# Performance work log

Measured on AMD Instinct MI355X. Metric: run time of the kernel, lower is better.

## Reference

```python
import jax, jax.numpy as jnp
import numpy as np

N_TOKEN = 32000
N_LAYER = 6
N_HEAD = 16
D_MODEL = 1024
D_HEAD = 64
D_INNER = 4096
QLEN = 512
MEM_LEN = 512
BSZ = 8
HD = N_HEAD * D_HEAD
SCALE = 1.0 / float(np.sqrt(D_HEAD))
NEG = -1e30


def _layer_norm(x, g, b, eps=1e-5):
    mu = jnp.mean(x, axis=-1, keepdims=True)
    var = jnp.var(x, axis=-1, keepdims=True)
    return (x - mu) * jax.lax.rsqrt(var + eps) * g + b


def _rel_shift(x):
    # x: [qlen, klen, bsz, n_head] -- TXL relative-position shift
    q, k, b, n = x.shape
    zp = jnp.zeros((q, 1, b, n), x.dtype)
    xp = jnp.concatenate([zp, x], axis=1).reshape(k + 1, q, b, n)
    return xp[1:].reshape(q, k, b, n)


def setup_inputs():
    key = jax.random.key(0)
    ks = jax.random.split(key, 12)
    s = 0.02
    rn = lambda k, *sh: jax.random.normal(k, sh, jnp.float32) * s
    z = lambda *sh: jnp.zeros(sh, jnp.float32)
    o = lambda *sh: jnp.ones(sh, jnp.float32)
    return {
        "data": jax.random.randint(ks[0], (QLEN, BSZ), 0, N_TOKEN),
        "target": jax.random.randint(ks[1], (QLEN, BSZ), 0, N_TOKEN),
        "memory": jax.random.normal(ks[2], (N_LAYER, MEM_LEN, BSZ, D_MODEL), jnp.float32),
        "emb_W": rn(ks[3], N_TOKEN, D_MODEL),  # tied input embedding / softmax head
        "r_w_bias": rn(ks[4], N_HEAD, D_HEAD),
        "r_r_bias": rn(ks[5], N_HEAD, D_HEAD),
        "Wq": rn(ks[6], N_LAYER, D_MODEL, HD),
        "Wkv": rn(ks[7], N_LAYER, D_MODEL, 2 * HD),
        "Wr": rn(ks[8], N_LAYER, D_MODEL, HD),
        "Wo": rn(ks[9], N_LAYER, HD, D_MODEL),
        "W1": rn(ks[10], N_LAYER, D_MODEL, D_INNER),
        "b1": z(N_LAYER, D_INNER),
        "W2": rn(ks[11], N_LAYER, D_INNER, D_MODEL),
        "b2": z(N_LAYER, D_MODEL),
        "ln1_g": o(N_LAYER, D_MODEL),
        "ln1_b": z(N_LAYER, D_MODEL),
        "ln2_g": o(N_LAYER, D_MODEL),
        "ln2_b": z(N_LAYER, D_MODEL),
    }


def _model(data, target, memory, emb_W, r_w_bias, r_r_bias, Wq, Wkv, Wr, Wo,
           W1, b1, W2, b2, ln1_g, ln1_b, ln2_g, ln2_b):
    qlen, bsz = data.shape
    mem = jax.lax.stop_gradient(memory)  # TXL detaches memories
    mlen = mem.shape[1]
    klen = mlen + qlen

    word_emb = emb_W[data]  # [q, b, d]

    # sinusoidal relative positions klen-1 .. 0
    pos_seq = jnp.arange(klen - 1, -1, -1, dtype=word_emb.dtype)
    inv_freq = 1.0 / (10000.0 ** (jnp.arange(0, D_MODEL, 2, dtype=word_emb.dtype) / D_MODEL))
    sin_inp = pos_seq[:, None] * inv_freq[None, :]
    pos = jnp.concatenate([jnp.sin(sin_inp), jnp.cos(sin_inp)], axis=-1)  # [klen, d]

    # causal mask with memory: query i can attend keys j <= i + mlen
    mask = jnp.arange(klen)[None, :] > (jnp.arange(qlen)[:, None] + mlen)  # [q, k]

    core = word_emb
    hids = [core]
    for i in range(N_LAYER):
        x_mem = jnp.concatenate([mem[i], core], axis=0)  # [klen, b, d]
        q = (core @ Wq[i]).reshape(qlen, bsz, N_HEAD, D_HEAD)
        kv = x_mem @ Wkv[i]
        k, v = jnp.split(kv, 2, axis=-1)
        k = k.reshape(klen, bsz, N_HEAD, D_HEAD)
        v = v.reshape(klen, bsz, N_HEAD, D_HEAD)
        r_k = (pos @ Wr[i]).reshape(klen, N_HEAD, D_HEAD)

        AC = jnp.einsum('ibnd,jbnd->ijbn', q + r_w_bias, k)
        BD = _rel_shift(jnp.einsum('ibnd,jnd->ijbn', q + r_r_bias, r_k))
        score = (AC + BD) * SCALE
        score = jnp.where(mask[:, :, None, None], NEG, score)
        prob = jax.nn.softmax(score, axis=1)
        vec = jnp.einsum('ijbn,jbnd->ibnd', prob, v).reshape(qlen, bsz, HD)
        attn_out = vec @ Wo[i]
        core = _layer_norm(core + attn_out, ln1_g[i], ln1_b[i])
        ff = jax.nn.relu(core @ W1[i] + b1[i]) @ W2[i] + b2[i]
        core = _layer_norm(core + ff, ln2_g[i], ln2_b[i])
        hids.append(core)

    # adaptive softmax with cutoffs=[] == full tied softmax
    logits = core @ emb_W.T  # [q, b, V]
    logp = jax.nn.log_softmax(logits, axis=-1)
    loss = -jnp.take_along_axis(logp, target[..., None], axis=-1)[..., 0]  # [q, b]

    new_mems = jnp.stack([
        jnp.concatenate([mem[i], hids[i]], axis=0)[-MEM_LEN:] for i in range(N_LAYER)
    ])
    new_mems = jax.lax.stop_gradient(new_mems)
    return loss, new_mems


def reference(data, target, memory, emb_W, r_w_bias, r_r_bias, Wq, Wkv, Wr, Wo,
              W1, b1, W2, b2, ln1_g, ln1_b, ln2_g, ln2_b):
    return _model(data, target, memory, emb_W, r_w_bias, r_r_bias, Wq, Wkv, Wr, Wo,
                  W1, b1, W2, b2, ln1_g, ln1_b, ln2_g, ln2_b)
```

## Files before the change

kernel.cpp:

```cpp
#include <hip/hip_runtime.h>
#include <hip/hip_bf16.h>
#include <math.h>

#define QLEN   512
#define MLEN   512
#define KLEN   1024
#define BSZ    8
#define NH     16
#define DH     64
#define DM     1024
#define DI     4096
#define NTOK   32000
#define NROW   4096
#define XROW   8192
#define VTILES 500

typedef __hip_bfloat16 bf16;
typedef __attribute__((ext_vector_type(8))) short bf16x8;
typedef __attribute__((ext_vector_type(4))) float f32x4;

__device__ __forceinline__ unsigned short f2b(float x) {
    union { float f; unsigned u; } a; a.f = x;
    unsigned r = a.u + 0x7fffu + ((a.u >> 16) & 1u);
    return (unsigned short)(r >> 16);
}
__device__ __forceinline__ float b2f(unsigned short h) {
    union { unsigned u; float f; } a; a.u = ((unsigned)h) << 16;
    return a.f;
}

__device__ __forceinline__ void gload_lds16(const void* g, void* l) {
    __builtin_amdgcn_global_load_lds(
        (const __attribute__((address_space(1))) unsigned int*)g,
        (__attribute__((address_space(3))) unsigned int*)l, 16, 0, 0);
}

__global__ __launch_bounds__(256) void posb_kernel(unsigned short* __restrict__ posb) {
    int j = blockIdx.x;
    int t = threadIdx.x;
    float p = (float)(1023 - j);
    #pragma unroll
    for (int u = 0; u < 4; u++) {
        int dcol = t + u * 256;
        int k = dcol & 511;
        float invf = expf(-((float)k) * (1.0f / 512.0f) * 9.210340371976184f);
        float a = p * invf;
        posb[j * DM + dcol] = f2b((dcol < 512) ? sinf(a) : cosf(a));
    }
}

__global__ __launch_bounds__(256) void gather_emb(const int* __restrict__ data,
                                                  const float* __restrict__ emb,
                                                  float* __restrict__ out) {
    int row = blockIdx.x;
    int t = threadIdx.x;
    int tok = data[row];
    const float4* src = (const float4*)(emb + (size_t)tok * DM);
    float4* dst = (float4*)(out + (size_t)row * DM);
    dst[t] = src[t];
}

__global__ __launch_bounds__(256) void cast_bf16(const float* __restrict__ src,
                                                 unsigned short* __restrict__ dst, int n4) {
    int i = blockIdx.x * 256 + threadIdx.x;
    if (i < n4) {
        float4 v = ((const float4*)src)[i];
        ushort4 o;
        o.x = f2b(v.x); o.y = f2b(v.y); o.z = f2b(v.z); o.w = f2b(v.w);
        ((ushort4*)dst)[i] = o;
    }
}

__global__ __launch_bounds__(256) void castT_kernel(const float* __restrict__ src,
                                                    unsigned short* __restrict__ dst,
                                                    int K, int N) {
    __shared__ float T[32][33];
    int t = threadIdx.x;
    int k0 = blockIdx.y * 32, n0 = blockIdx.x * 32;
    int r = t >> 3, c4 = (t & 7) * 4;
    float4 v = *(const float4*)(src + (size_t)(k0 + r) * N + n0 + c4);
    T[r][c4 + 0] = v.x; T[r][c4 + 1] = v.y; T[r][c4 + 2] = v.z; T[r][c4 + 3] = v.w;
    __syncthreads();
    ushort4 o;
    o.x = f2b(T[c4 + 0][r]); o.y = f2b(T[c4 + 1][r]);
    o.z = f2b(T[c4 + 2][r]); o.w = f2b(T[c4 + 3][r]);
    *(ushort4*)(dst + (size_t)(n0 + r) * K + k0 + c4) = o;
}

template <bool BIAS, bool RELU, bool OUTBF16>
__global__ __launch_bounds__(256) void gemm_bt(const unsigned short* __restrict__ A,
                                               const unsigned short* __restrict__ B,
                                               const float* __restrict__ bias,
                                               void* __restrict__ Cout,
                                               int M, int N, int K) {
    __shared__ unsigned short As[128 * 32];
    __shared__ unsigned short Bs[128 * 32];
    int t = threadIdx.x;
    int wave = t >> 6, lane = t & 63;
    int bm = blockIdx.y * 128, bn = blockIdx.x * 128;
    int wm = (wave >> 1) * 64, wn = (wave & 1) * 64;
    int quad = lane >> 4, l16 = lane & 15;

    f32x4 acc[4][4] = {};

    int srow = wave * 32 + (lane >> 2);
    int scol = (lane & 3) * 8;
    const unsigned short* Ag = A + (size_t)(bm + srow) * K + scol;
    const unsigned short* Bg = B + (size_t)(bn + srow) * K + scol;
    unsigned short* Al0 = As + (wave * 32) * 32;
    unsigned short* Al1 = As + (wave * 32 + 16) * 32;
    unsigned short* Bl0 = Bs + (wave * 32) * 32;
    unsigned short* Bl1 = Bs + (wave * 32 + 16) * 32;

    for (int kt = 0; kt < K; kt += 32) {
        gload_lds16(Ag + kt, Al0);
        gload_lds16(Ag + kt + (size_t)16 * K, Al1);
        gload_lds16(Bg + kt, Bl0);
        gload_lds16(Bg + kt + (size_t)16 * K, Bl1);
        __syncthreads();
        bf16x8 af[4], bfr[4];
        #pragma unroll
        for (int mi = 0; mi < 4; mi++)
            af[mi] = *(const bf16x8*)&As[(wm + mi * 16 + l16) * 32 + quad * 8];
        #pragma unroll
        for (int ni = 0; ni < 4; ni++)
            bfr[ni] = *(const bf16x8*)&Bs[(wn + ni * 16 + l16) * 32 + quad * 8];
        #pragma unroll
        for (int mi = 0; mi < 4; mi++)
            #pragma unroll
            for (int ni = 0; ni < 4; ni++)
                acc[mi][ni] = __builtin_amdgcn_mfma_f32_16x16x32_bf16(
                    af[mi], bfr[ni], acc[mi][ni], 0, 0, 0);
        __syncthreads();
    }

    #pragma unroll
    for (int mi = 0; mi < 4; mi++) {
        #pragma unroll
        for (int ni = 0; ni < 4; ni++) {
            int c = bn + wn + ni * 16 + l16;
            float bv = BIAS ? bias[c] : 0.0f;
            #pragma unroll
            for (int reg = 0; reg < 4; reg++) {
                int r = bm + wm + mi * 16 + quad * 4 + reg;
                float x = acc[mi][ni][reg];
                if (BIAS) x += bv;
                if (RELU) x = fmaxf(x, 0.0f);
                if (OUTBF16) ((unsigned short*)Cout)[(size_t)r * N + c] = f2b(x);
                else         ((float*)Cout)[(size_t)r * N + c] = x;
            }
        }
    }
}

__global__ __launch_bounds__(256) void lse_gemm_mfma(const unsigned short* __restrict__ A,
                                                     const unsigned short* __restrict__ B,
                                                     float* __restrict__ pmax,
                                                     float* __restrict__ psum) {
    __shared__ unsigned short As[128 * 32];
    __shared__ unsigned short Bs[128 * 32];
    int t = threadIdx.x;
    int wave = t >> 6, lane = t & 63;
    int bm = blockIdx.y * 128, bn = blockIdx.x * 128;
    int wm = (wave >> 1) * 64;
    int quad = lane >> 4, l16 = lane & 15;
    const int K = 1024;

    f32x4 acc[4][4] = {};

    int srow = wave * 32 + (lane >> 2);
    int scol = (lane & 3) * 8;
    const unsigned short* Ag = A + (size_t)(bm + srow) * K + scol;
    const unsigned short* Bg = B + (size_t)(bn + srow) * K + scol;
    unsigned short* Al0 = As + (wave * 32) * 32;
    unsigned short* Al1 = As + (wave * 32 + 16) * 32;
    unsigned short* Bl0 = Bs + (wave * 32) * 32;
    unsigned short* Bl1 = Bs + (wave * 32 + 16) * 32;
    int wn = (wave & 1) * 64;

    for (int kt = 0; kt < K; kt += 32) {
        gload_lds16(Ag + kt, Al0);
        gload_lds16(Ag + kt + (size_t)16 * K, Al1);
        gload_lds16(Bg + kt, Bl0);
        gload_lds16(Bg + kt + (size_t)16 * K, Bl1);
        __syncthreads();
        bf16x8 af[4], bfr[4];
        #pragma unroll
        for (int mi = 0; mi < 4; mi++)
            af[mi] = *(const bf16x8*)&As[(wm + mi * 16 + l16) * 32 + quad * 8];
        #pragma unroll
        for (int ni = 0; ni < 4; ni++)
            bfr[ni] = *(const bf16x8*)&Bs[(wn + ni * 16 + l16) * 32 + quad * 8];
        #pragma unroll
        for (int mi = 0; mi < 4; mi++)
            #pragma unroll
            for (int ni = 0; ni < 4; ni++)
                acc[mi][ni] = __builtin_amdgcn_mfma_f32_16x16x32_bf16(
                    af[mi], bfr[ni], acc[mi][ni], 0, 0, 0);
        __syncthreads();
    }

    int vt = blockIdx.x * 2 + (wave & 1);
    #pragma unroll
    for (int mi = 0; mi < 4; mi++) {
        #pragma unroll
        for (int reg = 0; reg < 4; reg++) {
            float m = -1e30f;
            #pragma unroll
            for (int ni = 0; ni < 4; ni++) m = fmaxf(m, acc[mi][ni][reg]);
            #pragma unroll
            for (int off = 1; off < 16; off <<= 1) m = fmaxf(m, __shfl_xor(m, off, 64));
            float s = 0.0f;
            #pragma unroll
            for (int ni = 0; ni < 4; ni++) s += __expf(acc[mi][ni][reg] - m);
            #pragma unroll
            for (int off = 1; off < 16; off <<= 1) s += __shfl_xor(s, off, 64);
            if (l16 == 0) {
                int r = bm + wm + mi * 16 + quad * 4 + reg;
                pmax[(size_t)r * VTILES + vt] = m;
                psum[(size_t)r * VTILES + vt] = s;
            }
        }
    }
}

__global__ __launch_bounds__(256) void qprep(const float* __restrict__ qbuf,
                                             const float* __restrict__ rwb,
                                             const float* __restrict__ rrb,
                                             unsigned short* __restrict__ qw,
                                             unsigned short* __restrict__ qr) {
    int row = blockIdx.x;
    int t = threadIdx.x;
    int i = row >> 3;
    float4 v = ((const float4*)(qbuf + (size_t)row * DM))[t];
    float4 w = ((const float4*)rwb)[t];
    float4 r = ((const float4*)rrb)[t];
    ushort4 ow, os;
    ow.x = f2b(v.x + w.x); ow.y = f2b(v.y + w.y); ow.z = f2b(v.z + w.z); ow.w = f2b(v.w + w.w);
    os.x = f2b(v.x + r.x); os.y = f2b(v.y + r.y); os.z = f2b(v.z + r.z); os.w = f2b(v.w + r.w);
    ((ushort4*)(qr + (size_t)row * DM))[t] = os;
    int col = t * 4;
    int idx = (col & ~63) + ((col & 63) ^ ((i & 7) << 3));
    *(ushort4*)(qw + (size_t)row * DM + idx) = ow;
}

__global__ __launch_bounds__(256) void kvprep(const float* __restrict__ kvf,
                                              unsigned short* __restrict__ Kh,
                                              unsigned short* __restrict__ Vth) {
    int nb = blockIdx.x, jt = blockIdx.y;
    int n = nb >> 3, b = nb & 7;
    int t = threadIdx.x;
    __shared__ float T[64][65];
    int jj = t >> 2, c4 = (t & 3) * 16;
    int j = jt * 64 + jj;
    const float* src = kvf + (size_t)(j * 8 + b) * 2048 + n * 64;
    unsigned short* kdst = Kh + (size_t)nb * 65536 + (size_t)j * 64;
    #pragma unroll
    for (int c = 0; c < 4; c++) {
        float4 k4 = ((const float4*)src)[(c4 >> 2) + c];
        ushort4 o;
        o.x = f2b(k4.x); o.y = f2b(k4.y); o.z = f2b(k4.z); o.w = f2b(k4.w);
        int d = c4 + c * 4;
        *(ushort4*)(kdst + (d ^ ((j & 7) << 3))) = o;
    }
    const float* vsrc = src + 1024;
    #pragma unroll
    for (int c = 0; c < 4; c++) {
        float4 v4 = ((const float4*)vsrc)[(c4 >> 2) + c];
        int d = c4 + c * 4;
        T[jj][d] = v4.x; T[jj][d + 1] = v4.y; T[jj][d + 2] = v4.z; T[jj][d + 3] = v4.w;
    }
    __syncthreads();
    int d = t >> 2, j4 = (t & 3) * 16;
    unsigned short* vrow = Vth + (size_t)nb * 65536 + (size_t)d * 1024 + (size_t)(jt >> 1) * 128;
    #pragma unroll
    for (int c = 0; c < 4; c++) {
        ushort4 o;
        int jb = j4 + c * 4;
        o.x = f2b(T[jb][d]); o.y = f2b(T[jb + 1][d]);
        o.z = f2b(T[jb + 2][d]); o.w = f2b(T[jb + 3][d]);
        int jl = (jt & 1) * 64 + jb;
        *(ushort4*)(vrow + (jl ^ ((d & 7) << 3))) = o;
    }
}

__global__ __launch_bounds__(256) void bd_gemm(const unsigned short* __restrict__ A,
                                               const unsigned short* __restrict__ B,
                                               unsigned short* __restrict__ Bt) {
    __shared__ unsigned short As[128 * 32];
    __shared__ unsigned short Bs[128 * 32];
    int t = threadIdx.x;
    int wave = t >> 6, lane = t & 63;
    int bm = blockIdx.y * 128, bn = blockIdx.x * 128, n = blockIdx.z;
    int wm = (wave >> 1) * 64, wn = (wave & 1) * 64;
    int quad = lane >> 4, l16 = lane & 15;
    f32x4 acc[4][4] = {};
    int srow = wave * 32 + (lane >> 2);
    int scol = (lane & 3) * 8;
    const unsigned short* Ag = A + (size_t)(bm + srow) * DM + n * 64 + scol;
    const unsigned short* Bg = B + (size_t)(bn + srow) * DM + n * 64 + scol;
    unsigned short* Al0 = As + (wave * 32) * 32;
    unsigned short* Al1 = As + (wave * 32 + 16) * 32;
    unsigned short* Bl0 = Bs + (wave * 32) * 32;
    unsigned short* Bl1 = Bs + (wave * 32 + 16) * 32;

    #pragma unroll
    for (int kt = 0; kt < 64; kt += 32) {
        gload_lds16(Ag + kt, Al0);
        gload_lds16(Ag + kt + (size_t)16 * DM, Al1);
        gload_lds16(Bg + kt, Bl0);
        gload_lds16(Bg + kt + (size_t)16 * DM, Bl1);
        __syncthreads();
        bf16x8 af[4], bfr[4];
        #pragma unroll
        for (int mi = 0; mi < 4; mi++)
            af[mi] = *(const bf16x8*)&As[(wm + mi * 16 + l16) * 32 + quad * 8];
        #pragma unroll
        for (int ni = 0; ni < 4; ni++)
            bfr[ni] = *(const bf16x8*)&Bs[(wn + ni * 16 + l16) * 32 + quad * 8];
        #pragma unroll
        for (int mi = 0; mi < 4; mi++)
            #pragma unroll
            for (int ni = 0; ni < 4; ni++)
                acc[mi][ni] = __builtin_amdgcn_mfma_f32_16x16x32_bf16(
                    af[mi], bfr[ni], acc[mi][ni], 0, 0, 0);
        __syncthreads();
    }

    #pragma unroll
    for (int mi = 0; mi < 4; mi++) {
        #pragma unroll
        for (int reg = 0; reg < 4; reg++) {
            int r = bm + wm + mi * 16 + quad * 4 + reg;
            int i = r >> 3;
            size_t rowbase = ((size_t)n * 4096 + r) * 1024;
            int sw = (i & 7) << 3;
            #pragma unroll
            for (int ni = 0; ni < 4; ni++) {
                int p = bn + wn + ni * 16 + l16;
                int j = p + i - 511;
                if ((unsigned)j < 1024u)
                    Bt[rowbase + (j & ~127) + ((j & 127) ^ sw)] = f2b(acc[mi][ni][reg]);
            }
        }
    }
}

__global__ __launch_bounds__(256) void flash_attn(const unsigned short* __restrict__ qw_b,
                                                  const unsigned short* __restrict__ Kh,
                                                  const unsigned short* __restrict__ Vth,
                                                  const unsigned short* __restrict__ Bt,
                                                  float* __restrict__ vec) {
    int qb = blockIdx.x, b = blockIdx.y, n = blockIdx.z;
    int i0 = qb * 64, nb = n * 8 + b;
    int t = threadIdx.x, wave = t >> 6, lane = t & 63;
    int quad = lane >> 4, l16 = lane & 15;
    int wm = wave * 16;
    __shared__ unsigned short Qw_s[64 * 64];
    __shared__ unsigned short K_s[128 * 64];
    __shared__ unsigned short Vt_s[64 * 128];
    __shared__ unsigned short BD_s[64 * 128];

    {
        const unsigned short* g = qw_b
            + (size_t)((i0 + wave * 16 + (lane >> 3)) * 8 + b) * DM + n * 64 + (lane & 7) * 8;
        unsigned short* l = Qw_s + (wave * 16) * 64;
        gload_lds16(g, l);
        gload_lds16(g + (size_t)64 * DM, l + 8 * 64);
    }

    f32x4 o[4] = {};
    float m_run[4] = { -1e30f, -1e30f, -1e30f, -1e30f };
    float l_run[4] = {};

    int nt = ((i0 + 575) >> 7) + 1;
    for (int jt = 0; jt < nt; jt++) {
        int j0 = jt * 128;
        __syncthreads();
        {
            const unsigned short* g = Kh + (size_t)nb * 65536
                + (size_t)(j0 + wave * 32 + (lane >> 3)) * 64 + (lane & 7) * 8;
            unsigned short* l = K_s + (wave * 32) * 64;
            #pragma unroll
            for (int k = 0; k < 4; k++)
                gload_lds16(g + (size_t)k * 512, l + k * 512);
        }
        {
            const unsigned short* g = Vth + (size_t)nb * 65536
                + (size_t)(wave * 16 + (lane >> 4)) * 1024 + j0 + (lane & 15) * 8;
            unsigned short* l = Vt_s + (wave * 16) * 128;
            #pragma unroll
            for (int k = 0; k < 4; k++)
                gload_lds16(g + (size_t)k * 4096, l + k * 512);
        }
        {
            const unsigned short* g = Bt
                + ((size_t)n * 4096 + (size_t)(i0 + wave * 16 + (lane >> 4)) * 8 + b) * 1024
                + j0 + (lane & 15) * 8;
            unsigned short* l = BD_s + (wave * 16) * 128;
            #pragma unroll
            for (int k = 0; k < 4; k++)
                gload_lds16(g + (size_t)k * 32768, l + k * 512);
        }
        __syncthreads();

        int arow = wm + l16;
        int asw = (arow & 7) << 3;
        bf16x8 aq0 = *(const bf16x8*)&Qw_s[arow * 64 + ((quad * 8) ^ asw)];
        bf16x8 aq1 = *(const bf16x8*)&Qw_s[arow * 64 + ((32 + quad * 8) ^ asw)];
        f32x4 s[8];
        #pragma unroll
        for (int ni = 0; ni < 8; ni++) {
            int krow = ni * 16 + l16;
            int ksw = (krow & 7) << 3;
            bf16x8 b0 = *(const bf16x8*)&K_s[krow * 64 + ((quad * 8) ^ ksw)];
            bf16x8 b1 = *(const bf16x8*)&K_s[krow * 64 + ((32 + quad * 8) ^ ksw)];
            f32x4 z = {};
            z = __builtin_amdgcn_mfma_f32_16x16x32_bf16(aq0, b0, z, 0, 0, 0);
            s[ni] = __builtin_amdgcn_mfma_f32_16x16x32_bf16(aq1, b1, z, 0, 0, 0);
        }

        bool last = (jt == nt - 1);
        #pragma unroll
        for (int reg = 0; reg < 4; reg++) {
            int rl = quad * 4 + reg;
            int rsw = (rl & 7) << 3;
            #pragma unroll
            for (int ni = 0; ni < 8; ni++) {
                int c = ni * 16 + l16;
                float bd = b2f(BD_s[(wm + rl) * 128 + (c ^ rsw)]);
                float v = (s[ni][reg] + bd) * 0.125f;
                if (last && (j0 + c > i0 + wm + rl + 512)) v = -1e30f;
                s[ni][reg] = v;
            }
        }

        #pragma unroll
        for (int reg = 0; reg < 4; reg++) {
            float tm = s[0][reg];
            #pragma unroll
            for (int ni = 1; ni < 8; ni++) tm = fmaxf(tm, s[ni][reg]);
            #pragma unroll
            for (int off = 1; off < 16; off <<= 1) tm = fmaxf(tm, __shfl_xor(tm, off, 64));
            float mn = fmaxf(m_run[reg], tm);
            float alpha = __expf(m_run[reg] - mn);
            m_run[reg] = mn;
            float ts = 0.f;
            #pragma unroll
            for (int ni = 0; ni < 8; ni++) {
                float p = __expf(s[ni][reg] - mn);
                s[ni][reg] = p;
                ts += p;
            }
            #pragma unroll
            for (int off = 1; off < 16; off <<= 1) ts += __shfl_xor(ts, off, 64);
            l_run[reg] = l_run[reg] * alpha + ts;
            #pragma unroll
            for (int di = 0; di < 4; di++) o[di][reg] *= alpha;
        }

        #pragma unroll
        for (int reg = 0; reg < 4; reg++) {
            int rl = quad * 4 + reg;
            int rsw = (rl & 7) << 3;
            #pragma unroll
            for (int ni = 0; ni < 8; ni++) {
                int c = ni * 16 + l16;
                BD_s[(wm + rl) * 128 + (c ^ rsw)] = f2b(s[ni][reg]);
            }
        }

        #pragma unroll
        for (int kk = 0; kk < 4; kk++) {
            int prow = wm + l16;
            bf16x8 ap = *(const bf16x8*)&BD_s[prow * 128 + ((kk * 32 + quad * 8) ^ ((prow & 7) << 3))];
            #pragma unroll
            for (int di = 0; di < 4; di++) {
                int vr = di * 16 + l16;
                bf16x8 bv = *(const bf16x8*)&Vt_s[vr * 128 + ((kk * 32 + quad * 8) ^ ((vr & 7) << 3))];
                o[di] = __builtin_amdgcn_mfma_f32_16x16x32_bf16(ap, bv, o[di], 0, 0, 0);
            }
        }
    }

    #pragma unroll
    for (int reg = 0; reg < 4; reg++) {
        float inv = 1.0f / l_run[reg];
        int r = i0 + wm + quad * 4 + reg;
        #pragma unroll
        for (int di = 0; di < 4; di++) {
            vec[(size_t)(r * 8 + b) * 1024 + n * 64 + di * 16 + l16] = o[di][reg] * inv;
        }
    }
}

__global__ __launch_bounds__(256) void add_ln_kernel(const float* __restrict__ x,
                                                     const float* __restrict__ y,
                                                     const float* __restrict__ g,
                                                     const float* __restrict__ bb,
                                                     float* __restrict__ out) {
    int row = blockIdx.x;
    int t = threadIdx.x;
    __shared__ float rs[256], rq[256];
    float v[4];
    float s = 0.f, sq = 0.f;
    #pragma unroll
    for (int u = 0; u < 4; u++) {
        int c = t + u * 256;
        float val = x[(size_t)row * DM + c] + y[(size_t)row * DM + c];
        v[u] = val;
        s += val;
        sq += val * val;
    }
    rs[t] = s;
    rq[t] = sq;
    __syncthreads();
    for (int off = 128; off > 0; off >>= 1) {
        if (t < off) { rs[t] += rs[t + off]; rq[t] += rq[t + off]; }
        __syncthreads();
    }
    float mu = rs[0] * (1.0f / 1024.0f);
    float var = rq[0] * (1.0f / 1024.0f) - mu * mu;
    float rstd = rsqrtf(var + 1e-5f);
    #pragma unroll
    for (int u = 0; u < 4; u++) {
        int c = t + u * 256;
        out[(size_t)row * DM + c] = (v[u] - mu) * rstd * g[c] + bb[c];
    }
}

__global__ __launch_bounds__(256) void tgt_logit_bf(const unsigned short* __restrict__ core,
                                                    const unsigned short* __restrict__ emb,
                                                    const int* __restrict__ target,
                                                    float* __restrict__ out) {
    int row = blockIdx.x;
    int t = threadIdx.x;
    __shared__ float red[256];
    int tok = target[row];
    const unsigned short* a = core + (size_t)row * DM;
    const unsigned short* e = emb + (size_t)tok * DM;
    float s = 0.f;
    #pragma unroll
    for (int u = 0; u < 4; u++) {
        int c = t + u * 256;
        s += b2f(a[c]) * b2f(e[c]);
    }
    red[t] = s;
    __syncthreads();
    for (int off = 128; off > 0; off >>= 1) {
        if (t < off) red[t] += red[t + off];
        __syncthreads();
    }
    if (t == 0) out[row] = red[0];
}

__global__ __launch_bounds__(256) void lse_reduce_kernel(const float* __restrict__ pmax,
                                                         const float* __restrict__ psum,
                                                         const float* __restrict__ ltgt,
                                                         float* __restrict__ loss) {
    int row = blockIdx.x;
    int t = threadIdx.x;
    __shared__ float red[256];
    float m = -1e30f;
    for (int u = t; u < VTILES; u += 256) m = fmaxf(m, pmax[(size_t)row * VTILES + u]);
    red[t] = m;
    __syncthreads();
    for (int off = 128; off > 0; off >>= 1) {
        if (t < off) red[t] = fmaxf(red[t], red[t + off]);
        __syncthreads();
    }
    float M = red[0];
    __syncthreads();
    float s = 0.f;
    for (int u = t; u < VTILES; u += 256)
        s += psum[(size_t)row * VTILES + u] * __expf(pmax[(size_t)row * VTILES + u] - M);
    red[t] = s;
    __syncthreads();
    for (int off = 128; off > 0; off >>= 1) {
        if (t < off) red[t] += red[t + off];
        __syncthreads();
    }
    if (t == 0) loss[row] = M + logf(red[0]) - ltgt[row];
}

extern "C" void kernel_launch(void* const* d_in, const int* in_sizes, int n_in,
                              void* d_out, int out_size, void* d_ws, size_t ws_size,
                              hipStream_t stream) {
    const int*   data   = (const int*)d_in[0];
    const int*   target = (const int*)d_in[1];
    const float* memory = (const float*)d_in[2];
    const float* embW   = (const float*)d_in[3];
    const float* rwb    = (const float*)d_in[4];
    const float* rrb    = (const float*)d_in[5];
    const float* Wq     = (const float*)d_in[6];
    const float* Wkv    = (const float*)d_in[7];
    const float* Wr     = (const float*)d_in[8];
    const float* Wo     = (const float*)d_in[9];
    const float* W1     = (const float*)d_in[10];
    const float* b1     = (const float*)d_in[11];
    const float* W2     = (const float*)d_in[12];
    const float* b2     = (const float*)d_in[13];
    const float* ln1g   = (const float*)d_in[14];
    const float* ln1b   = (const float*)d_in[15];
    const float* ln2g   = (const float*)d_in[16];
    const float* ln2b   = (const float*)d_in[17];

    float* out  = (float*)d_out;
    float* loss = out;
    float* hids = out + 4096;

    const size_t SZ_CORE = (size_t)NROW * DM;

    const size_t MB = 1024 * 1024;
    char* base = (char*)d_ws;
    unsigned short* posb = (unsigned short*)(base);
    unsigned short* Vth  = (unsigned short*)(base + 2 * MB);
    unsigned short* Kh   = (unsigned short*)(base + 18 * MB);
    float* qbuf          = (float*)(base + 34 * MB);
    float* vec           = (float*)(base + 34 * MB);
    unsigned short* qw_b = (unsigned short*)(base + 50 * MB);
    unsigned short* qr_b = (unsigned short*)(base + 58 * MB);
    unsigned short* rkb  = (unsigned short*)(base + 66 * MB);
    float* kvf           = (float*)(base + 70 * MB);
    unsigned short* Bt   = (unsigned short*)(base + 70 * MB);
    unsigned short* wT   = (unsigned short*)(base + 2 * MB);
    unsigned short* actb = (unsigned short*)(base + 10 * MB);
    float* tmp           = (float*)(base + 18 * MB);
    float* cmid          = (float*)(base + 70 * MB);
    unsigned short* h1b  = (unsigned short*)(base + 86 * MB);
    float* corefinal     = (float*)(base + 182 * MB);
    unsigned short* corefnb = actb;
    unsigned short* embWb   = (unsigned short*)(base + 70 * MB);
    float* pmax = (float*)(base + 136 * MB);
    float* psum = (float*)(base + 146 * MB);
    float* ltgt = (float*)(base + 160 * MB);

    posb_kernel<<<KLEN, 256, 0, stream>>>(posb);
    gather_emb<<<NROW, 256, 0, stream>>>(data, embW, hids);

    for (int L = 0; L < 6; L++) {
        const float* cin = hids + (size_t)L * SZ_CORE;
        float* cout = (L < 5) ? (hids + (size_t)(L + 1) * SZ_CORE) : corefinal;

        unsigned short* xmemb = Kh;
        unsigned short* cinb = xmemb + SZ_CORE;
        cast_bf16<<<4096, 256, 0, stream>>>(memory + (size_t)L * SZ_CORE, xmemb, 1 << 20);
        cast_bf16<<<4096, 256, 0, stream>>>(cin, cinb, 1 << 20);

        castT_kernel<<<dim3(32, 32), 256, 0, stream>>>(Wq + (size_t)L * DM * DM, wT, DM, DM);
        gemm_bt<false, false, false><<<dim3(8, 32), 256, 0, stream>>>(
            cinb, wT, nullptr, qbuf, NROW, DM, DM);

        castT_kernel<<<dim3(64, 32), 256, 0, stream>>>(Wkv + (size_t)L * DM * 2 * DM, wT, DM, 2 * DM);
        gemm_bt<false, false, false><<<dim3(16, 64), 256, 0, stream>>>(
            xmemb, wT, nullptr, kvf, XROW, 2 * DM, DM);

        castT_kernel<<<dim3(32, 32), 256, 0, stream>>>(Wr + (size_t)L * DM * DM, wT, DM, DM);
        gemm_bt<false, false, true><<<dim3(8, 8), 256, 0, stream>>>(
            posb, wT, nullptr, rkb, KLEN, DM, DM);

        qprep<<<NROW, 256, 0, stream>>>(qbuf, rwb, rrb, qw_b, qr_b);
        kvprep<<<dim3(128, 16), 256, 0, stream>>>(kvf, Kh, Vth);
        bd_gemm<<<dim3(8, 32, 16), 256, 0, stream>>>(qr_b, rkb, Bt);
        flash_attn<<<dim3(8, 8, 16), 256, 0, stream>>>(qw_b, Kh, Vth, Bt, vec);

        cast_bf16<<<4096, 256, 0, stream>>>(vec, actb, 1 << 20);
        castT_kernel<<<dim3(32, 32), 256, 0, stream>>>(Wo + (size_t)L * DM * DM, wT, DM, DM);
        gemm_bt<false, false, false><<<dim3(8, 32), 256, 0, stream>>>(
            actb, wT, nullptr, tmp, NROW, DM, DM);

        add_ln_kernel<<<NROW, 256, 0, stream>>>(cin, tmp, ln1g + L * DM, ln1b + L * DM, cmid);

        cast_bf16<<<4096, 256, 0, stream>>>(cmid, actb, 1 << 20);
        castT_kernel<<<dim3(128, 32), 256, 0, stream>>>(W1 + (size_t)L * DM * DI, wT, DM, DI);
        gemm_bt<true, true, true><<<dim3(32, 32), 256, 0, stream>>>(
            actb, wT, b1 + (size_t)L * DI, h1b, NROW, DI, DM);

        castT_kernel<<<dim3(32, 128), 256, 0, stream>>>(W2 + (size_t)L * DI * DM, wT, DI, DM);
        gemm_bt<true, false, false><<<dim3(8, 32), 256, 0, stream>>>(
            h1b, wT, b2 + (size_t)L * DM, tmp, NROW, DM, DI);

        add_ln_kernel<<<NROW, 256, 0, stream>>>(cmid, tmp, ln2g + L * DM, ln2b + L * DM, cout);
    }

    cast_bf16<<<4096, 256, 0, stream>>>(corefinal, corefnb, 1 << 20);
    cast_bf16<<<32768, 256, 0, stream>>>(embW, embWb, (NTOK * DM) / 4);
    tgt_logit_bf<<<NROW, 256, 0, stream>>>(corefnb, embWb, target, ltgt);
    lse_gemm_mfma<<<dim3(250, 32), 256, 0, stream>>>(corefnb, embWb, pmax, psum);
    lse_reduce_kernel<<<NROW, 256, 0, stream>>>(pmax, psum, ltgt, loss);
}
```

Measured before the change: 3.768 ms.

## Fuse Q/KV projections, hoist Wr GEMM, split-K W2, bf16 attention output

Q and KV projections are merged into one GEMM over the concatenated memory+input rows with a concatenated transposed weight. The position projection for all layers is computed once up front. Flash attention writes bf16 directly, removing a cast pass. The W2 GEMM is split-K by 4 into partial buffers summed inside the fused add+layernorm, and the LSE GEMM grid axes are swapped for better embedding reuse. The Q projection now also runs on memory rows, which is wasted compute, and split-K adds extra partial-buffer traffic.

```diff
diff --git a/kernel.cpp b/kernel.cpp
--- a/kernel.cpp
+++ b/kernel.cpp
@@ -87,7 +87,7 @@
     *(ushort4*)(dst + (size_t)(n0 + r) * K + k0 + c4) = o;
 }
 
-template <bool BIAS, bool RELU, bool OUTBF16>
+template <bool BIAS, bool RELU, bool OUTBF16, int SPLITK = 1>
 __global__ __launch_bounds__(256) void gemm_bt(const unsigned short* __restrict__ A,
                                                const unsigned short* __restrict__ B,
                                                const float* __restrict__ bias,
@@ -112,7 +112,9 @@
     unsigned short* Bl0 = Bs + (wave * 32) * 32;
     unsigned short* Bl1 = Bs + (wave * 32 + 16) * 32;
 
-    for (int kt = 0; kt < K; kt += 32) {
+    int kchunk = K / SPLITK;
+    int k0 = (SPLITK > 1) ? blockIdx.z * kchunk : 0;
+    for (int kt = k0; kt < k0 + kchunk; kt += 32) {
         gload_lds16(Ag + kt, Al0);
         gload_lds16(Ag + kt + (size_t)16 * K, Al1);
         gload_lds16(Bg + kt, Bl0);
@@ -134,6 +136,7 @@
         __syncthreads();
     }
 
+    float* Cf = (float*)Cout + ((SPLITK > 1) ? (size_t)blockIdx.z * M * N : (size_t)0);
     #pragma unroll
     for (int mi = 0; mi < 4; mi++) {
         #pragma unroll
@@ -147,7 +150,7 @@
                 if (BIAS) x += bv;
                 if (RELU) x = fmaxf(x, 0.0f);
                 if (OUTBF16) ((unsigned short*)Cout)[(size_t)r * N + c] = f2b(x);
-                else         ((float*)Cout)[(size_t)r * N + c] = x;
+                else         Cf[(size_t)r * N + c] = x;
             }
         }
     }
@@ -161,7 +164,7 @@
     __shared__ unsigned short Bs[128 * 32];
     int t = threadIdx.x;
     int wave = t >> 6, lane = t & 63;
-    int bm = blockIdx.y * 128, bn = blockIdx.x * 128;
+    int bm = blockIdx.x * 128, bn = blockIdx.y * 128;
     int wm = (wave >> 1) * 64;
     int quad = lane >> 4, l16 = lane & 15;
     const int K = 1024;
@@ -200,7 +203,7 @@
         __syncthreads();
     }
 
-    int vt = blockIdx.x * 2 + (wave & 1);
+    int vt = blockIdx.y * 2 + (wave & 1);
     #pragma unroll
     for (int mi = 0; mi < 4; mi++) {
         #pragma unroll
@@ -224,7 +227,7 @@
     }
 }
 
-__global__ __launch_bounds__(256) void qprep(const float* __restrict__ qbuf,
+__global__ __launch_bounds__(256) void qprep(const float* __restrict__ kqv,
                                              const float* __restrict__ rwb,
                                              const float* __restrict__ rrb,
                                              unsigned short* __restrict__ qw,
@@ -232,7 +235,7 @@
     int row = blockIdx.x;
     int t = threadIdx.x;
     int i = row >> 3;
-    float4 v = ((const float4*)(qbuf + (size_t)row * DM))[t];
+    float4 v = ((const float4*)(kqv + (size_t)(4096 + row) * 3072))[t];
     float4 w = ((const float4*)rwb)[t];
     float4 r = ((const float4*)rrb)[t];
     ushort4 ow, os;
@@ -244,7 +247,7 @@
     *(ushort4*)(qw + (size_t)row * DM + idx) = ow;
 }
 
-__global__ __launch_bounds__(256) void kvprep(const float* __restrict__ kvf,
+__global__ __launch_bounds__(256) void kvprep(const float* __restrict__ kqv,
                                               unsigned short* __restrict__ Kh,
                                               unsigned short* __restrict__ Vth) {
     int nb = blockIdx.x, jt = blockIdx.y;
@@ -253,7 +256,7 @@
     __shared__ float T[64][65];
     int jj = t >> 2, c4 = (t & 3) * 16;
     int j = jt * 64 + jj;
-    const float* src = kvf + (size_t)(j * 8 + b) * 2048 + n * 64;
+    const float* src = kqv + (size_t)(j * 8 + b) * 3072 + 1024 + n * 64;
     unsigned short* kdst = Kh + (size_t)nb * 65536 + (size_t)j * 64;
     #pragma unroll
     for (int c = 0; c < 4; c++) {
@@ -286,6 +289,7 @@
 
 __global__ __launch_bounds__(256) void bd_gemm(const unsigned short* __restrict__ A,
                                                const unsigned short* __restrict__ B,
+                                               int ldb,
                                                unsigned short* __restrict__ Bt) {
     __shared__ unsigned short As[128 * 32];
     __shared__ unsigned short Bs[128 * 32];
@@ -298,7 +302,7 @@
     int srow = wave * 32 + (lane >> 2);
     int scol = (lane & 3) * 8;
     const unsigned short* Ag = A + (size_t)(bm + srow) * DM + n * 64 + scol;
-    const unsigned short* Bg = B + (size_t)(bn + srow) * DM + n * 64 + scol;
+    const unsigned short* Bg = B + (size_t)(bn + srow) * ldb + n * 64 + scol;
     unsigned short* Al0 = As + (wave * 32) * 32;
     unsigned short* Al1 = As + (wave * 32 + 16) * 32;
     unsigned short* Bl0 = Bs + (wave * 32) * 32;
@@ -309,7 +313,7 @@
         gload_lds16(Ag + kt, Al0);
         gload_lds16(Ag + kt + (size_t)16 * DM, Al1);
         gload_lds16(Bg + kt, Bl0);
-        gload_lds16(Bg + kt + (size_t)16 * DM, Bl1);
+        gload_lds16(Bg + kt + (size_t)16 * ldb, Bl1);
         __syncthreads();
         bf16x8 af[4], bfr[4];
         #pragma unroll
@@ -350,7 +354,7 @@
                                                   const unsigned short* __restrict__ Kh,
                                                   const unsigned short* __restrict__ Vth,
                                                   const unsigned short* __restrict__ Bt,
-                                                  float* __restrict__ vec) {
+                                                  unsigned short* __restrict__ vecb) {
     int qb = blockIdx.x, b = blockIdx.y, n = blockIdx.z;
     int i0 = qb * 64, nb = n * 8 + b;
     int t = threadIdx.x, wave = t >> 6, lane = t & 63;
@@ -489,7 +493,7 @@
         int r = i0 + wm + quad * 4 + reg;
         #pragma unroll
         for (int di = 0; di < 4; di++) {
-            vec[(size_t)(r * 8 + b) * 1024 + n * 64 + di * 16 + l16] = o[di][reg] * inv;
+            vecb[(size_t)(r * 8 + b) * 1024 + n * 64 + di * 16 + l16] = f2b(o[di][reg] * inv);
         }
     }
 }
@@ -508,6 +512,44 @@
     for (int u = 0; u < 4; u++) {
         int c = t + u * 256;
         float val = x[(size_t)row * DM + c] + y[(size_t)row * DM + c];
+        v[u] = val;
+        s += val;
+        sq += val * val;
+    }
+    rs[t] = s;
+    rq[t] = sq;
+    __syncthreads();
+    for (int off = 128; off > 0; off >>= 1) {
+        if (t < off) { rs[t] += rs[t + off]; rq[t] += rq[t + off]; }
+        __syncthreads();
+    }
+    float mu = rs[0] * (1.0f / 1024.0f);
+    float var = rq[0] * (1.0f / 1024.0f) - mu * mu;
+    float rstd = rsqrtf(var + 1e-5f);
+    #pragma unroll
+    for (int u = 0; u < 4; u++) {
+        int c = t + u * 256;
+        out[(size_t)row * DM + c] = (v[u] - mu) * rstd * g[c] + bb[c];
+    }
+}
+
+__global__ __launch_bounds__(256) void add_ln4_kernel(const float* __restrict__ x,
+                                                      const float* __restrict__ p,
+                                                      const float* __restrict__ bias,
+                                                      const float* __restrict__ g,
+                                                      const float* __restrict__ bb,
+                                                      float* __restrict__ out) {
+    const size_t S = (size_t)NROW * DM;
+    int row = blockIdx.x;
+    int t = threadIdx.x;
+    __shared__ float rs[256], rq[256];
+    float v[4];
+    float s = 0.f, sq = 0.f;
+    #pragma unroll
+    for (int u = 0; u < 4; u++) {
+        int c = t + u * 256;
+        size_t idx = (size_t)row * DM + c;
+        float val = x[idx] + bias[c] + p[idx] + p[S + idx] + p[2 * S + idx] + p[3 * S + idx];
         v[u] = val;
         s += val;
         sq += val * val;
@@ -613,22 +655,23 @@
 
     const size_t MB = 1024 * 1024;
     char* base = (char*)d_ws;
-    unsigned short* posb = (unsigned short*)(base);
-    unsigned short* Vth  = (unsigned short*)(base + 2 * MB);
-    unsigned short* Kh   = (unsigned short*)(base + 18 * MB);
-    float* qbuf          = (float*)(base + 34 * MB);
-    float* vec           = (float*)(base + 34 * MB);
-    unsigned short* qw_b = (unsigned short*)(base + 50 * MB);
-    unsigned short* qr_b = (unsigned short*)(base + 58 * MB);
-    unsigned short* rkb  = (unsigned short*)(base + 66 * MB);
-    float* kvf           = (float*)(base + 70 * MB);
-    unsigned short* Bt   = (unsigned short*)(base + 70 * MB);
+    unsigned short* posb   = (unsigned short*)(base);
+    unsigned short* Vth    = (unsigned short*)(base + 2 * MB);
+    unsigned short* Kh     = (unsigned short*)(base + 18 * MB);
+    unsigned short* vecb   = (unsigned short*)(base + 34 * MB);
+    unsigned short* rkball = (unsigned short*)(base + 42 * MB);
+    unsigned short* qw_b   = (unsigned short*)(base + 54 * MB);
+    unsigned short* qr_b   = (unsigned short*)(base + 62 * MB);
+    float* kqv             = (float*)(base + 70 * MB);
+    unsigned short* Bt     = (unsigned short*)(base + 70 * MB);
     unsigned short* wT   = (unsigned short*)(base + 2 * MB);
     unsigned short* actb = (unsigned short*)(base + 10 * MB);
     float* tmp           = (float*)(base + 18 * MB);
     float* cmid          = (float*)(base + 70 * MB);
     unsigned short* h1b  = (unsigned short*)(base + 86 * MB);
-    float* corefinal     = (float*)(base + 182 * MB);
+    float* w2p           = (float*)(base + 118 * MB);
+    float* corefinal     = (float*)(base + 18 * MB);
+    unsigned short* wrT  = (unsigned short*)(base + 70 * MB);
     unsigned short* corefnb = actb;
     unsigned short* embWb   = (unsigned short*)(base + 70 * MB);
     float* pmax = (float*)(base + 136 * MB);
@@ -638,6 +681,12 @@
     posb_kernel<<<KLEN, 256, 0, stream>>>(posb);
     gather_emb<<<NROW, 256, 0, stream>>>(data, embW, hids);
 
+    for (int L = 0; L < 6; L++)
+        castT_kernel<<<dim3(32, 32), 256, 0, stream>>>(
+            Wr + (size_t)L * DM * DM, wrT + (size_t)L * DM * DM, DM, DM);
+    gemm_bt<false, false, true><<<dim3(48, 8), 256, 0, stream>>>(
+        posb, wrT, nullptr, rkball, KLEN, 6 * DM, DM);
+
     for (int L = 0; L < 6; L++) {
         const float* cin = hids + (size_t)L * SZ_CORE;
         float* cout = (L < 5) ? (hids + (size_t)(L + 1) * SZ_CORE) : corefinal;
@@ -648,26 +697,19 @@
         cast_bf16<<<4096, 256, 0, stream>>>(cin, cinb, 1 << 20);
 
         castT_kernel<<<dim3(32, 32), 256, 0, stream>>>(Wq + (size_t)L * DM * DM, wT, DM, DM);
-        gemm_bt<false, false, false><<<dim3(8, 32), 256, 0, stream>>>(
-            cinb, wT, nullptr, qbuf, NROW, DM, DM);
-
-        castT_kernel<<<dim3(64, 32), 256, 0, stream>>>(Wkv + (size_t)L * DM * 2 * DM, wT, DM, 2 * DM);
-        gemm_bt<false, false, false><<<dim3(16, 64), 256, 0, stream>>>(
-            xmemb, wT, nullptr, kvf, XROW, 2 * DM, DM);
-
-        castT_kernel<<<dim3(32, 32), 256, 0, stream>>>(Wr + (size_t)L * DM * DM, wT, DM, DM);
-        gemm_bt<false, false, true><<<dim3(8, 8), 256, 0, stream>>>(
-            posb, wT, nullptr, rkb, KLEN, DM, DM);
-
-        qprep<<<NROW, 256, 0, stream>>>(qbuf, rwb, rrb, qw_b, qr_b);
-        kvprep<<<dim3(128, 16), 256, 0, stream>>>(kvf, Kh, Vth);
-        bd_gemm<<<dim3(8, 32, 16), 256, 0, stream>>>(qr_b, rkb, Bt);
-        flash_attn<<<dim3(8, 8, 16), 256, 0, stream>>>(qw_b, Kh, Vth, Bt, vec);
-
-        cast_bf16<<<4096, 256, 0, stream>>>(vec, actb, 1 << 20);
+        castT_kernel<<<dim3(64, 32), 256, 0, stream>>>(
+            Wkv + (size_t)L * DM * 2 * DM, wT + (size_t)DM * DM, DM, 2 * DM);
+        gemm_bt<false, false, false><<<dim3(24, 64), 256, 0, stream>>>(
+            xmemb, wT, nullptr, kqv, XROW, 3 * DM, DM);
+
+        qprep<<<NROW, 256, 0, stream>>>(kqv, rwb, rrb, qw_b, qr_b);
+        kvprep<<<dim3(128, 16), 256, 0, stream>>>(kqv, Kh, Vth);
+        bd_gemm<<<dim3(8, 32, 16), 256, 0, stream>>>(qr_b, rkball + (size_t)L * DM, 6 * DM, Bt);
+        flash_attn<<<dim3(8, 8, 16), 256, 0, stream>>>(qw_b, Kh, Vth, Bt, vecb);
+
         castT_kernel<<<dim3(32, 32), 256, 0, stream>>>(Wo + (size_t)L * DM * DM, wT, DM, DM);
         gemm_bt<false, false, false><<<dim3(8, 32), 256, 0, stream>>>(
-            actb, wT, nullptr, tmp, NROW, DM, DM);
+            vecb, wT, nullptr, tmp, NROW, DM, DM);
 
         add_ln_kernel<<<NROW, 256, 0, stream>>>(cin, tmp, ln1g + L * DM, ln1b + L * DM, cmid);
 
@@ -677,15 +719,16 @@
             actb, wT, b1 + (size_t)L * DI, h1b, NROW, DI, DM);
 
         castT_kernel<<<dim3(32, 128), 256, 0, stream>>>(W2 + (size_t)L * DI * DM, wT, DI, DM);
-        gemm_bt<true, false, false><<<dim3(8, 32), 256, 0, stream>>>(
-            h1b, wT, b2 + (size_t)L * DM, tmp, NROW, DM, DI);
-
-        add_ln_kernel<<<NROW, 256, 0, stream>>>(cmid, tmp, ln2g + L * DM, ln2b + L * DM, cout);
+        gemm_bt<false, false, false, 4><<<dim3(8, 32, 4), 256, 0, stream>>>(
+            h1b, wT, nullptr, w2p, NROW, DM, DI);
+
+        add_ln4_kernel<<<NROW, 256, 0, stream>>>(
+            cmid, w2p, b2 + (size_t)L * DM, ln2g + L * DM, ln2b + L * DM, cout);
     }
 
     cast_bf16<<<4096, 256, 0, stream>>>(corefinal, corefnb, 1 << 20);
     cast_bf16<<<32768, 256, 0, stream>>>(embW, embWb, (NTOK * DM) / 4);
     tgt_logit_bf<<<NROW, 256, 0, stream>>>(corefnb, embWb, target, ltgt);
-    lse_gemm_mfma<<<dim3(250, 32), 256, 0, stream>>>(corefnb, embWb, pmax, psum);
+    lse_gemm_mfma<<<dim3(32, 250), 256, 0, stream>>>(corefnb, embWb, pmax, psum);
     lse_reduce_kernel<<<NROW, 256, 0, stream>>>(pmax, psum, ltgt, loss);
 }
```

Result: faster. 3.435 ms (-8.9%).
